# Kernel optimization log

Measured on AMD Instinct MI355X. Metric: run time of the kernel, lower is better.

## Reference

```python
import jax, jax.numpy as jnp
import numpy as np

N = 100_000      # nodes
E = 3_200_000    # edges (avg degree 32)
H = 16           # hidden channels
C_IN, C_OUT = 1, 2


def setup_inputs() -> dict:
    key = jax.random.key(0)
    k1, k2, k3, k4, k5 = jax.random.split(key, 5)
    x = jax.random.normal(k1, (N, C_IN), dtype=jnp.float32)
    src = jax.random.randint(k2, (E,), 0, N, dtype=jnp.int32)
    dst = jax.random.randint(k3, (E,), 0, N, dtype=jnp.int32)
    edge_index = jnp.stack([src, dst])  # [2, E], PyG layout
    # Glorot-style init for the two linear transforms
    W1 = jax.random.normal(k4, (C_IN, H), dtype=jnp.float32) * np.sqrt(2.0 / (C_IN + H))
    b1 = jnp.zeros((H,), dtype=jnp.float32)
    W2 = jax.random.normal(k5, (H, C_OUT), dtype=jnp.float32) * np.sqrt(2.0 / (H + C_OUT))
    b2 = jnp.zeros((C_OUT,), dtype=jnp.float32)
    return {"x": x, "edge_index": edge_index, "W1": W1, "b1": b1, "W2": W2, "b2": b2}


def _gcn_conv(x, src, dst, W, b):
    """GCNConv: out = D^{-1/2} (A+I) D^{-1/2} X W + b.
    src/dst already include self-loops. x: [N, Cin], W: [Cin, Cout]."""
    deg = jax.ops.segment_sum(jnp.ones_like(dst, dtype=x.dtype), dst, num_segments=N)
    dinv = jnp.where(deg > 0, jax.lax.rsqrt(jnp.maximum(deg, 1.0)), 0.0)
    norm = dinv[src] * dinv[dst]                       # [E+N]
    h = x @ W                                          # transform first (Cin small)
    msg = norm[:, None] * h[src]                       # [E+N, Cout]
    out = jax.ops.segment_sum(msg, dst, num_segments=N)
    return out + b


def reference(x, edge_index, W1, b1, W2, b2):
    loops = jnp.arange(N, dtype=edge_index.dtype)
    src = jnp.concatenate([edge_index[0], loops])      # add self-loops
    dst = jnp.concatenate([edge_index[1], loops])
    h = _gcn_conv(x, src, dst, W1, b1)
    h = jax.nn.relu(h)
    out = _gcn_conv(h, src, dst, W2, b2)
    return out
```

## Files before the change

### kernel.cpp

```cpp
#include <hip/hip_runtime.h>

#define NN 100000
#define NE 3200000
#define HC 16

#define BKT_BITS 7
#define BKT_NODES 128
#define NB 782
#define NB1 783
#define CHUNK_S 4096
#define NCC2 782
#define NCCP 784
#define MCAP 5120
#define PADW (((unsigned)NN << BKT_BITS) | (BKT_NODES - 1))

typedef unsigned uv4 __attribute__((ext_vector_type(4)));
typedef int      iv4 __attribute__((ext_vector_type(4)));


__global__ __launch_bounds__(256) void k_sortchunk(const int* __restrict__ src,
                                                   const int* __restrict__ dst,
                                                   unsigned short* __restrict__ Hoff,
                                                   unsigned* __restrict__ binned) {
    __shared__ unsigned h[NB1];
    __shared__ unsigned sorted[CHUNK_S];
    __shared__ unsigned wsum[4];
    int tid = threadIdx.x;
    int c = blockIdx.x;
    int b0 = c * CHUNK_S;
    int e1 = min(b0 + CHUNK_S, NE);
    int cnt = e1 - b0;

    for (int j = tid; j < NB1; j += 256) h[j] = 0;
    __syncthreads();

    iv4 dreg[4], sreg[4];
    int nit = 0;
    for (int v = b0 + tid * 4; v + 3 < e1; v += 1024) {
        iv4 d4 = *(const iv4*)(dst + v);
        iv4 s4 = *(const iv4*)(src + v);
        dreg[nit] = d4; sreg[nit] = s4; ++nit;
        atomicAdd(&h[((unsigned)d4.x) >> BKT_BITS], 1u);
        atomicAdd(&h[((unsigned)d4.y) >> BKT_BITS], 1u);
        atomicAdd(&h[((unsigned)d4.z) >> BKT_BITS], 1u);
        atomicAdd(&h[((unsigned)d4.w) >> BKT_BITS], 1u);
    }
    __syncthreads();

    int i0 = tid * 4;
    unsigned v0 = (i0 + 0 < NB1) ? h[i0 + 0] : 0;
    unsigned v1 = (i0 + 1 < NB1) ? h[i0 + 1] : 0;
    unsigned v2 = (i0 + 2 < NB1) ? h[i0 + 2] : 0;
    unsigned v3 = (i0 + 3 < NB1) ? h[i0 + 3] : 0;
    unsigned lsum = v0 + v1 + v2 + v3;
    unsigned sc = lsum;
#pragma unroll
    for (int off = 1; off < 64; off <<= 1) {
        unsigned u = __shfl_up(sc, off, 64);
        if ((tid & 63) >= off) sc += u;
    }
    int wave = tid >> 6;
    if ((tid & 63) == 63) wsum[wave] = sc;
    __syncthreads();
    unsigned wpre = 0;
    for (int w = 0; w < wave; ++w) wpre += wsum[w];
    unsigned excl = wpre + sc - lsum;
    __syncthreads();
    if (i0 + 0 < NB1) h[i0 + 0] = excl;
    if (i0 + 1 < NB1) h[i0 + 1] = excl + v0;
    if (i0 + 2 < NB1) h[i0 + 2] = excl + v0 + v1;
    if (i0 + 3 < NB1) h[i0 + 3] = excl + v0 + v1 + v2;

    unsigned short* row = Hoff + (size_t)c * NB1;
    if (i0 + 0 < NB1) row[i0 + 0] = (unsigned short)excl;
    if (i0 + 1 < NB1) row[i0 + 1] = (unsigned short)(excl + v0);
    if (i0 + 2 < NB1) row[i0 + 2] = (unsigned short)(excl + v0 + v1);
    if (i0 + 3 < NB1) row[i0 + 3] = (unsigned short)(excl + v0 + v1 + v2);
    __syncthreads();

    int it = 0;
    for (int v = b0 + tid * 4; v + 3 < e1; v += 1024, ++it) {
        iv4 d4 = dreg[it];
        iv4 s4 = sreg[it];
        {   unsigned d = (unsigned)d4.x, s = (unsigned)s4.x;
            unsigned pos = atomicAdd(&h[d >> BKT_BITS], 1u);
            sorted[pos] = (s << BKT_BITS) | (d & (BKT_NODES - 1)); }
        {   unsigned d = (unsigned)d4.y, s = (unsigned)s4.y;
            unsigned pos = atomicAdd(&h[d >> BKT_BITS], 1u);
            sorted[pos] = (s << BKT_BITS) | (d & (BKT_NODES - 1)); }
        {   unsigned d = (unsigned)d4.z, s = (unsigned)s4.z;
            unsigned pos = atomicAdd(&h[d >> BKT_BITS], 1u);
            sorted[pos] = (s << BKT_BITS) | (d & (BKT_NODES - 1)); }
        {   unsigned d = (unsigned)d4.w, s = (unsigned)s4.w;
            unsigned pos = atomicAdd(&h[d >> BKT_BITS], 1u);
            sorted[pos] = (s << BKT_BITS) | (d & (BKT_NODES - 1)); }
    }
    __syncthreads();

    unsigned* out = binned + (size_t)c * CHUNK_S;
    for (int j = tid * 4; j + 3 < cnt; j += 1024)
        *(uv4*)(out + j) = *(const uv4*)(sorted + j);
}


__global__ __launch_bounds__(256) void k_transT(const unsigned short* __restrict__ Hoff,
                                                unsigned short* __restrict__ TH) {
    __shared__ unsigned short tile[32][33];
    int tx = threadIdx.x & 31;
    int ty0 = (threadIdx.x >> 5) * 4;
    int c0 = blockIdx.x * 32;
    int b0 = blockIdx.y * 32;
#pragma unroll
    for (int k = 0; k < 4; ++k) {
        int c = c0 + ty0 + k, b = b0 + tx;
        tile[ty0 + k][tx] = (c < NCC2 && b < NB1) ? Hoff[(size_t)c * NB1 + b] : (unsigned short)0;
    }
    __syncthreads();
#pragma unroll
    for (int k = 0; k < 4; ++k) {
        int b = b0 + ty0 + k, c = c0 + tx;
        if (b < NB1 && c < NCC2) TH[(size_t)b * NCCP + c] = tile[tx][ty0 + k];
    }
}


__global__ __launch_bounds__(64) void k_totals(const unsigned short* __restrict__ TH,
                                               unsigned* __restrict__ totals) {
    int b = blockIdx.x;
    int lane = threadIdx.x;
    const unsigned short* r0 = TH + (size_t)b * NCCP;
    const unsigned short* r1 = r0 + NCCP;
    unsigned s = 0;
    for (int c = lane; c < NCC2; c += 64) s += (unsigned)r1[c] - (unsigned)r0[c];
#pragma unroll
    for (int off = 32; off >= 1; off >>= 1) s += __shfl_xor(s, off, 64);
    if (lane == 0) totals[b] = s;
}

__global__ __launch_bounds__(1024) void k_base2(const unsigned* __restrict__ totals,
                                                unsigned* __restrict__ gbase) {
    __shared__ unsigned s[1024];
    int t = threadIdx.x;
    unsigned v = (t < NB) ? ((totals[t] + 15u) & ~15u) : 0;
    s[t] = v;
    __syncthreads();
    for (int off = 1; off < 1024; off <<= 1) {
        unsigned u = (t >= off) ? s[t - off] : 0;
        __syncthreads();
        s[t] += u;
        __syncthreads();
    }
    if (t < NB) gbase[t] = s[t] - v;
}


__global__ __launch_bounds__(256) void k_merge_deg(const unsigned* __restrict__ binned,
                                                   const unsigned short* __restrict__ TH,
                                                   const unsigned* __restrict__ gbase,
                                                   const float* __restrict__ x,
                                                   unsigned* __restrict__ merged,
                                                   unsigned short* __restrict__ cofsg,
                                                   float* __restrict__ dinv,
                                                   float* __restrict__ p) {
    __shared__ unsigned short th0s[NCC2];
    __shared__ unsigned short lens[NCC2];
    __shared__ unsigned S[NB1];
    __shared__ unsigned wsum[4];
    __shared__ unsigned cnt[BKT_NODES];
    __shared__ unsigned stage[MCAP];
    __shared__ unsigned short cof[BKT_NODES + 2];
    __shared__ unsigned wsA;
    int tid = threadIdx.x, b = blockIdx.x;

    const unsigned short* r0 = TH + (size_t)b * NCCP;
    const unsigned short* r1 = r0 + NCCP;
    for (int c = tid; c < NCC2; c += 256) {
        unsigned a = r0[c];
        th0s[c] = (unsigned short)a;
        lens[c] = (unsigned short)((unsigned)r1[c] - a);
    }
    if (tid < BKT_NODES) cnt[tid] = 0;
    __syncthreads();

    int i0 = tid * 4;
    unsigned v0 = (i0 + 0 < NCC2) ? (unsigned)lens[i0 + 0] : 0;
    unsigned v1 = (i0 + 1 < NCC2) ? (unsigned)lens[i0 + 1] : 0;
    unsigned v2 = (i0 + 2 < NCC2) ? (unsigned)lens[i0 + 2] : 0;
    unsigned v3 = (i0 + 3 < NCC2) ? (unsigned)lens[i0 + 3] : 0;
    unsigned lsum = v0 + v1 + v2 + v3;
    unsigned sc = lsum;
#pragma unroll
    for (int off = 1; off < 64; off <<= 1) {
        unsigned u = __shfl_up(sc, off, 64);
        if ((tid & 63) >= off) sc += u;
    }
    int wave = tid >> 6;
    if ((tid & 63) == 63) wsum[wave] = sc;
    __syncthreads();
    unsigned wpre = 0;
    for (int w = 0; w < wave; ++w) wpre += wsum[w];
    unsigned excl = wpre + sc - lsum;
    if (i0 + 0 <= NCC2) S[i0 + 0] = excl;
    if (i0 + 1 <= NCC2) S[i0 + 1] = excl + v0;
    if (i0 + 2 <= NCC2) S[i0 + 2] = excl + v0 + v1;
    if (i0 + 3 <= NCC2) S[i0 + 3] = excl + v0 + v1 + v2;
    __syncthreads();

    unsigned T = S[NCC2];
    unsigned Tr = (T + 15u) & ~15u;
    unsigned gb = gbase[b];
    if (tid < 16) {
        unsigned q = T + tid;
        if (q < Tr) stage[q] = PADW;
    }

    for (int c = tid; c < NCC2; c += 256) {
        unsigned off = th0s[c], L = lens[c];
        if (!L) continue;
        unsigned base = S[c];
        const unsigned* segbase = binned + (size_t)c * CHUNK_S;
        unsigned je = off + L;
        for (unsigned j4 = off & ~3u; j4 < je; j4 += 4) {
            uv4 e4 = *(const uv4*)(segbase + j4);
#pragma unroll
            for (int k = 0; k < 4; ++k) {
                unsigned j = j4 + (unsigned)k;
                if (j >= off && j < je) {
                    unsigned e = ((const unsigned*)&e4)[k];
                    atomicAdd(&cnt[e & (BKT_NODES - 1)], 1u);
                    stage[base + (j - off)] = e;
                }
            }
        }
    }
    __syncthreads();

    for (unsigned j = tid * 4; j < Tr; j += 1024)
        *(uv4*)(merged + gb + j) = *(const uv4*)(stage + j);

    unsigned cv = (tid < BKT_NODES) ? cnt[tid] : 0u;
    unsigned csc = cv;
#pragma unroll
    for (int off = 1; off < 64; off <<= 1) {
        unsigned u = __shfl_up(csc, off, 64);
        if ((tid & 63) >= off) csc += u;
    }
    if (tid == 63) wsA = csc;
    __syncthreads();
    if (tid < BKT_NODES) {
        unsigned incl = csc + ((tid >= 64) ? wsA : 0u);
        cof[tid + 1] = (unsigned short)incl;
    }
    if (tid == 0) cof[0] = 0;
    __syncthreads();
    if (tid < BKT_NODES + 1)
        cofsg[(size_t)b * (BKT_NODES + 2) + tid] = cof[tid];

    int node = b * BKT_NODES + tid;
    if (tid < BKT_NODES) {
        if (node < NN) {
            float di = rsqrtf((float)(cnt[tid] + 1u));
            dinv[node] = di;
            p[node] = di * x[node];
        } else if (node == NN) {
            p[node] = 0.f;
        }
    }
}


__global__ __launch_bounds__(256) void k_agg1(const unsigned* __restrict__ merged,
                                              const unsigned* __restrict__ gbase,
                                              const unsigned* __restrict__ totals,
                                              const unsigned short* __restrict__ cofsg,
                                              const float* __restrict__ dinv,
                                              const float* __restrict__ p,
                                              const float* __restrict__ W1,
                                              const float* __restrict__ b1,
                                              const float* __restrict__ W2,
                                              float2* __restrict__ g) {
    __shared__ unsigned short cof[BKT_NODES + 2];
    __shared__ unsigned cur[BKT_NODES + 1];
    __shared__ unsigned se[MCAP];
    __shared__ float part[256];
    int tid = threadIdx.x, b = blockIdx.x;
    if (tid < BKT_NODES + 1) cof[tid] = cofsg[(size_t)b * (BKT_NODES + 2) + tid];
    __syncthreads();
    if (tid < BKT_NODES + 1) cur[tid] = cof[tid];
    __syncthreads();
    unsigned Tr = (totals[b] + 15u) & ~15u;
    const unsigned* m = merged + gbase[b];
    for (unsigned j = tid * 4; j < Tr; j += 1024) {
        uv4 e = *(const uv4*)(m + j);
        { unsigned w = e.x; unsigned sl = (w >> BKT_BITS >= NN) ? 128u : (w & (BKT_NODES - 1));
          se[atomicAdd(&cur[sl], 1u)] = w >> BKT_BITS; }
        { unsigned w = e.y; unsigned sl = (w >> BKT_BITS >= NN) ? 128u : (w & (BKT_NODES - 1));
          se[atomicAdd(&cur[sl], 1u)] = w >> BKT_BITS; }
        { unsigned w = e.z; unsigned sl = (w >> BKT_BITS >= NN) ? 128u : (w & (BKT_NODES - 1));
          se[atomicAdd(&cur[sl], 1u)] = w >> BKT_BITS; }
        { unsigned w = e.w; unsigned sl = (w >> BKT_BITS >= NN) ? 128u : (w & (BKT_NODES - 1));
          se[atomicAdd(&cur[sl], 1u)] = w >> BKT_BITS; }
    }
    __syncthreads();

    int nl = tid >> 1, half = tid & 1;
    unsigned o0 = cof[nl], o1 = cof[nl + 1];
    unsigned len = o1 - o0, mid = o0 + ((len + 1) >> 1);
    unsigned s = half ? mid : o0;
    unsigned e = half ? o1 : mid;
    float sum = 0.f;
    unsigned i = s;
    for (; i + 3 < e; i += 4) {
        unsigned a0 = se[i], a1 = se[i + 1], a2 = se[i + 2], a3 = se[i + 3];
        float x0 = p[a0], x1 = p[a1], x2 = p[a2], x3 = p[a3];
        sum += (x0 + x1) + (x2 + x3);
    }
    for (; i < e; ++i) sum += p[se[i]];
    part[tid] = sum;
    __syncthreads();

    if (!half) {
        int node = b * BKT_NODES + nl;
        if (node < NN) {
            float di = dinv[node];
            float sf = di * (part[tid] + part[tid + 1] + p[node]);
            float g0 = 0.f, g1 = 0.f;
#pragma unroll
            for (int c = 0; c < HC; ++c) {
                float h = fmaxf(fmaf(sf, W1[c], b1[c]), 0.f);
                g0 = fmaf(h, W2[2 * c], g0);
                g1 = fmaf(h, W2[2 * c + 1], g1);
            }
            g[node] = make_float2(di * g0, di * g1);
        }
    }
}


__global__ __launch_bounds__(256) void k_agg2(const unsigned* __restrict__ merged,
                                              const unsigned* __restrict__ gbase,
                                              const unsigned* __restrict__ totals,
                                              const unsigned short* __restrict__ cofsg,
                                              const float* __restrict__ dinv,
                                              const float2* __restrict__ g,
                                              const float* __restrict__ b2,
                                              float2* __restrict__ out) {
    __shared__ unsigned short cof[BKT_NODES + 2];
    __shared__ unsigned cur[BKT_NODES + 1];
    __shared__ unsigned se[MCAP];
    __shared__ float2 part[256];
    int tid = threadIdx.x, b = blockIdx.x;
    if (tid < BKT_NODES + 1) cof[tid] = cofsg[(size_t)b * (BKT_NODES + 2) + tid];
    __syncthreads();
    if (tid < BKT_NODES + 1) cur[tid] = cof[tid];
    __syncthreads();
    unsigned Tr = (totals[b] + 15u) & ~15u;
    const unsigned* m = merged + gbase[b];
    for (unsigned j = tid * 4; j < Tr; j += 1024) {
        uv4 e = *(const uv4*)(m + j);
        { unsigned w = e.x; unsigned sl = (w >> BKT_BITS >= NN) ? 128u : (w & (BKT_NODES - 1));
          se[atomicAdd(&cur[sl], 1u)] = w >> BKT_BITS; }
        { unsigned w = e.y; unsigned sl = (w >> BKT_BITS >= NN) ? 128u : (w & (BKT_NODES - 1));
          se[atomicAdd(&cur[sl], 1u)] = w >> BKT_BITS; }
        { unsigned w = e.z; unsigned sl = (w >> BKT_BITS >= NN) ? 128u : (w & (BKT_NODES - 1));
          se[atomicAdd(&cur[sl], 1u)] = w >> BKT_BITS; }
        { unsigned w = e.w; unsigned sl = (w >> BKT_BITS >= NN) ? 128u : (w & (BKT_NODES - 1));
          se[atomicAdd(&cur[sl], 1u)] = w >> BKT_BITS; }
    }
    __syncthreads();

    int nl = tid >> 1, half = tid & 1;
    unsigned o0 = cof[nl], o1 = cof[nl + 1];
    unsigned len = o1 - o0, mid = o0 + ((len + 1) >> 1);
    unsigned s = half ? mid : o0;
    unsigned e = half ? o1 : mid;
    float sx = 0.f, sy = 0.f;
    unsigned i = s;
    for (; i + 3 < e; i += 4) {
        unsigned a0 = se[i], a1 = se[i + 1], a2 = se[i + 2], a3 = se[i + 3];
        float2 v0 = g[a0], v1 = g[a1], v2 = g[a2], v3 = g[a3];
        sx += (v0.x + v1.x) + (v2.x + v3.x);
        sy += (v0.y + v1.y) + (v2.y + v3.y);
    }
    for (; i < e; ++i) { float2 v = g[se[i]]; sx += v.x; sy += v.y; }
    part[tid] = make_float2(sx, sy);
    __syncthreads();

    if (!half) {
        int node = b * BKT_NODES + nl;
        if (node < NN) {
            float di = dinv[node];
            float2 me = g[node];
            float ax = part[tid].x + part[tid + 1].x + me.x;
            float ay = part[tid].y + part[tid + 1].y + me.y;
            out[node] = make_float2(fmaf(di, ax, b2[0]), fmaf(di, ay, b2[1]));
        }
    }
}


__global__ __launch_bounds__(256) void f_deg(const int* __restrict__ dst,
                                             unsigned int* __restrict__ deg, int E) {
    int i = blockIdx.x * blockDim.x + threadIdx.x;
    if (i < E) atomicAdd(&deg[dst[i]], 1u);
}
__global__ __launch_bounds__(256) void f_node1(const float* __restrict__ x,
                                               const unsigned int* __restrict__ deg,
                                               float* __restrict__ dinv, float* __restrict__ p,
                                               float* __restrict__ t, int N) {
    int i = blockIdx.x * blockDim.x + threadIdx.x;
    if (i < N) {
        float di = rsqrtf((float)(deg[i] + 1u));
        dinv[i] = di; float pi = di * x[i]; p[i] = pi; t[i] = pi;
    }
}
__global__ __launch_bounds__(256) void f_scatter1(const int* __restrict__ src,
                                                  const int* __restrict__ dst,
                                                  const float* __restrict__ p,
                                                  float* __restrict__ t, int E) {
    int i = blockIdx.x * blockDim.x + threadIdx.x;
    if (i < E) atomicAdd(&t[dst[i]], p[src[i]]);
}
__global__ __launch_bounds__(256) void f_node2(const float* __restrict__ dinv,
                                               const float* __restrict__ t,
                                               const float* __restrict__ W1,
                                               const float* __restrict__ b1,
                                               const float* __restrict__ W2,
                                               float2* __restrict__ g,
                                               float2* __restrict__ acc, int N) {
    int i = blockIdx.x * blockDim.x + threadIdx.x;
    if (i < N) {
        float di = dinv[i]; float s = di * t[i];
        float g0 = 0.f, g1 = 0.f;
#pragma unroll
        for (int c = 0; c < HC; ++c) {
            float h = fmaxf(fmaf(s, W1[c], b1[c]), 0.f);
            g0 = fmaf(h, W2[2 * c], g0); g1 = fmaf(h, W2[2 * c + 1], g1);
        }
        float2 gv = make_float2(di * g0, di * g1);
        g[i] = gv; acc[i] = gv;
    }
}
__global__ __launch_bounds__(256) void f_scatter2(const int* __restrict__ src,
                                                  const int* __restrict__ dst,
                                                  const float2* __restrict__ g,
                                                  float* __restrict__ acc, int E) {
    int i = blockIdx.x * blockDim.x + threadIdx.x;
    if (i < E) {
        int s = src[i], d = dst[i];
        float2 gv = g[s];
        atomicAdd(&acc[2 * d], gv.x);
        atomicAdd(&acc[2 * d + 1], gv.y);
    }
}
__global__ __launch_bounds__(256) void f_out(const float* __restrict__ dinv,
                                             const float* __restrict__ b2,
                                             float* __restrict__ out, int N) {
    int i = blockIdx.x * blockDim.x + threadIdx.x;
    if (i < N) {
        float di = dinv[i];
        out[2 * i]     = fmaf(di, out[2 * i],     b2[0]);
        out[2 * i + 1] = fmaf(di, out[2 * i + 1], b2[1]);
    }
}

extern "C" void kernel_launch(void* const* d_in, const int* in_sizes, int n_in,
                              void* d_out, int out_size, void* d_ws, size_t ws_size,
                              hipStream_t stream) {
    const float* x  = (const float*)d_in[0];
    const int* ei   = (const int*)d_in[1];
    const int* src  = ei;
    const int* dst  = ei + NE;
    const float* W1 = (const float*)d_in[2];
    const float* b1 = (const float*)d_in[3];
    const float* W2 = (const float*)d_in[4];
    const float* b2 = (const float*)d_in[5];

    const int BT = 256;
    const int gridE = (NE + BT - 1) / BT;
    const int gridN = (NN + BT - 1) / BT;

    size_t need = 0;
    auto carve = [&](size_t bytes) { size_t o = need; need += (bytes + 255) & ~(size_t)255; return o; };
    size_t o_Hoff = carve((size_t)NCC2 * NB1 * 2);
    size_t o_TH   = carve((size_t)NB1 * NCCP * 2);
    size_t o_tot  = carve((size_t)NB * 4);
    size_t o_gb   = carve((size_t)(NB + 1) * 4);
    size_t o_cofs = carve((size_t)NB * (BKT_NODES + 2) * 2);
    size_t o_dinv = carve((size_t)NN * 4);
    size_t o_p    = carve((size_t)(NN + 1) * 4);
    size_t o_g    = carve((size_t)(NN + 1) * 8);
    size_t o_bin  = carve((size_t)NCC2 * CHUNK_S * 4);
    size_t o_mrg  = carve((size_t)(NE + 16 * NB + 64) * 4);

    if (ws_size >= need) {
        char* ws = (char*)d_ws;
        unsigned short* Hoff = (unsigned short*)(ws + o_Hoff);
        unsigned short* TH   = (unsigned short*)(ws + o_TH);
        unsigned* totals = (unsigned*)(ws + o_tot);
        unsigned* gbase  = (unsigned*)(ws + o_gb);
        unsigned short* cofs = (unsigned short*)(ws + o_cofs);
        float*    dinv   = (float*)(ws + o_dinv);
        float*    p      = (float*)(ws + o_p);
        float2*   g      = (float2*)(ws + o_g);
        unsigned* binned = (unsigned*)(ws + o_bin);
        unsigned* merged = (unsigned*)(ws + o_mrg);

        k_sortchunk<<<NCC2, 256, 0, stream>>>(src, dst, Hoff, binned);
        k_transT   <<<dim3(25, 25), 256, 0, stream>>>(Hoff, TH);
        k_totals   <<<NB, 64, 0, stream>>>(TH, totals);
        k_base2    <<<1, 1024, 0, stream>>>(totals, gbase);
        k_merge_deg<<<NB, 256, 0, stream>>>(binned, TH, gbase, x, merged, cofs, dinv, p);
        k_agg1     <<<NB, 256, 0, stream>>>(merged, gbase, totals, cofs, dinv, p, W1, b1, W2, g);
        k_agg2     <<<NB, 256, 0, stream>>>(merged, gbase, totals, cofs, dinv, g, b2, (float2*)d_out);
    } else {
        float* out = (float*)d_out;
        char* ws = (char*)d_ws;
        unsigned int* deg = (unsigned int*)ws;
        float* dinv = (float*)(ws + 1 * sizeof(float) * NN);
        float* p    = (float*)(ws + 2 * sizeof(float) * NN);
        float* t    = (float*)(ws + 3 * sizeof(float) * NN);
        float2* g   = (float2*)(ws + 4 * sizeof(float) * NN);

        hipMemsetAsync(deg, 0, NN * sizeof(unsigned int), stream);
        f_deg<<<gridE, BT, 0, stream>>>(dst, deg, NE);
        f_node1<<<gridN, BT, 0, stream>>>(x, deg, dinv, p, t, NN);
        f_scatter1<<<gridE, BT, 0, stream>>>(src, dst, p, t, NE);
        f_node2<<<gridN, BT, 0, stream>>>(dinv, t, W1, b1, W2, g, (float2*)out, NN);
        f_scatter2<<<gridE, BT, 0, stream>>>(src, dst, g, out, NE);
        f_out<<<gridN, BT, 0, stream>>>(dinv, b2, out, NN);
    }
}
```

Baseline: 155.4 us.

## Fuse both aggregation layers into one cooperative kernel with grid sync

Merges k_agg1 and k_agg2 into a single cooperative kernel. The per-bucket edge list is rebuilt into shared memory once and reused for both layers, with a grid-wide sync between them. This removes one kernel launch and the second pass that rebuilds se from merged. It relies on all 782 blocks being co-resident, and it falls back to the two-kernel path if the cooperative launch fails. The atomic-based fallback for small workspaces is removed, and g[NN] is now zeroed.

```diff
diff --git a/kernel.cpp b/kernel.cpp
--- a/kernel.cpp
+++ b/kernel.cpp
@@ -1,4 +1,7 @@
 #include <hip/hip_runtime.h>
+#include <hip/hip_cooperative_groups.h>
+
+namespace cg = cooperative_groups;
 
 #define NN 100000
 #define NE 3200000
@@ -269,6 +272,108 @@
 }
 
 
+__global__ __launch_bounds__(256) void k_agg12(const unsigned* __restrict__ merged,
+                                               const unsigned* __restrict__ gbase,
+                                               const unsigned* __restrict__ totals,
+                                               const unsigned short* __restrict__ cofsg,
+                                               const float* __restrict__ dinv,
+                                               const float* __restrict__ p,
+                                               const float* __restrict__ W1,
+                                               const float* __restrict__ b1,
+                                               const float* __restrict__ W2,
+                                               float2* __restrict__ g,
+                                               const float* __restrict__ b2,
+                                               float2* __restrict__ out) {
+    cg::grid_group grid = cg::this_grid();
+    __shared__ unsigned short cof[BKT_NODES + 2];
+    __shared__ unsigned cur[BKT_NODES + 1];
+    __shared__ unsigned se[MCAP];
+    __shared__ float part[256];
+    __shared__ float2 part2[256];
+    int tid = threadIdx.x, b = blockIdx.x;
+    if (tid < BKT_NODES + 1) cof[tid] = cofsg[(size_t)b * (BKT_NODES + 2) + tid];
+    __syncthreads();
+    if (tid < BKT_NODES + 1) cur[tid] = cof[tid];
+    __syncthreads();
+    unsigned Tr = (totals[b] + 15u) & ~15u;
+    const unsigned* m = merged + gbase[b];
+    for (unsigned j = tid * 4; j < Tr; j += 1024) {
+        uv4 e = *(const uv4*)(m + j);
+        { unsigned w = e.x; unsigned sl = (w >> BKT_BITS >= NN) ? 128u : (w & (BKT_NODES - 1));
+          se[atomicAdd(&cur[sl], 1u)] = w >> BKT_BITS; }
+        { unsigned w = e.y; unsigned sl = (w >> BKT_BITS >= NN) ? 128u : (w & (BKT_NODES - 1));
+          se[atomicAdd(&cur[sl], 1u)] = w >> BKT_BITS; }
+        { unsigned w = e.z; unsigned sl = (w >> BKT_BITS >= NN) ? 128u : (w & (BKT_NODES - 1));
+          se[atomicAdd(&cur[sl], 1u)] = w >> BKT_BITS; }
+        { unsigned w = e.w; unsigned sl = (w >> BKT_BITS >= NN) ? 128u : (w & (BKT_NODES - 1));
+          se[atomicAdd(&cur[sl], 1u)] = w >> BKT_BITS; }
+    }
+    __syncthreads();
+
+    int nl = tid >> 1, half = tid & 1;
+    unsigned o0 = cof[nl], o1 = cof[nl + 1];
+    unsigned len = o1 - o0, mid = o0 + ((len + 1) >> 1);
+    unsigned s = half ? mid : o0;
+    unsigned e = half ? o1 : mid;
+
+    {
+        float sum = 0.f;
+        unsigned i = s;
+        for (; i + 3 < e; i += 4) {
+            unsigned a0 = se[i], a1 = se[i + 1], a2 = se[i + 2], a3 = se[i + 3];
+            float x0 = p[a0], x1 = p[a1], x2 = p[a2], x3 = p[a3];
+            sum += (x0 + x1) + (x2 + x3);
+        }
+        for (; i < e; ++i) sum += p[se[i]];
+        part[tid] = sum;
+    }
+    __syncthreads();
+    if (!half) {
+        int node = b * BKT_NODES + nl;
+        if (node < NN) {
+            float di = dinv[node];
+            float sf = di * (part[tid] + part[tid + 1] + p[node]);
+            float g0 = 0.f, g1 = 0.f;
+#pragma unroll
+            for (int c = 0; c < HC; ++c) {
+                float h = fmaxf(fmaf(sf, W1[c], b1[c]), 0.f);
+                g0 = fmaf(h, W2[2 * c], g0);
+                g1 = fmaf(h, W2[2 * c + 1], g1);
+            }
+            g[node] = make_float2(di * g0, di * g1);
+        } else if (node == NN) {
+            g[node] = make_float2(0.f, 0.f);
+        }
+    }
+
+    grid.sync();
+
+    {
+        float sx = 0.f, sy = 0.f;
+        unsigned i = s;
+        for (; i + 3 < e; i += 4) {
+            unsigned a0 = se[i], a1 = se[i + 1], a2 = se[i + 2], a3 = se[i + 3];
+            float2 v0 = g[a0], v1 = g[a1], v2 = g[a2], v3 = g[a3];
+            sx += (v0.x + v1.x) + (v2.x + v3.x);
+            sy += (v0.y + v1.y) + (v2.y + v3.y);
+        }
+        for (; i < e; ++i) { float2 v = g[se[i]]; sx += v.x; sy += v.y; }
+        part2[tid] = make_float2(sx, sy);
+    }
+    __syncthreads();
+    if (!half) {
+        int node = b * BKT_NODES + nl;
+        if (node < NN) {
+            float di = dinv[node];
+            float2 me = g[node];
+            float ax = part2[tid].x + part2[tid + 1].x + me.x;
+            float ay = part2[tid].y + part2[tid + 1].y + me.y;
+            out[node] = make_float2(fmaf(di, ax, b2[0]), fmaf(di, ay, b2[1]));
+        }
+    }
+}
+
+
 __global__ __launch_bounds__(256) void k_agg1(const unsigned* __restrict__ merged,
                                               const unsigned* __restrict__ gbase,
                                               const unsigned* __restrict__ totals,
@@ -332,10 +437,11 @@
                 g1 = fmaf(h, W2[2 * c + 1], g1);
             }
             g[node] = make_float2(di * g0, di * g1);
-        }
-    }
-}
-
+        } else if (node == NN) {
+            g[node] = make_float2(0.f, 0.f);
+        }
+    }
+}
 
 __global__ __launch_bounds__(256) void k_agg2(const unsigned* __restrict__ merged,
                                               const unsigned* __restrict__ gbase,
@@ -398,72 +504,6 @@
     }
 }
 
-
-__global__ __launch_bounds__(256) void f_deg(const int* __restrict__ dst,
-                                             unsigned int* __restrict__ deg, int E) {
-    int i = blockIdx.x * blockDim.x + threadIdx.x;
-    if (i < E) atomicAdd(&deg[dst[i]], 1u);
-}
-__global__ __launch_bounds__(256) void f_node1(const float* __restrict__ x,
-                                               const unsigned int* __restrict__ deg,
-                                               float* __restrict__ dinv, float* __restrict__ p,
-                                               float* __restrict__ t, int N) {
-    int i = blockIdx.x * blockDim.x + threadIdx.x;
-    if (i < N) {
-        float di = rsqrtf((float)(deg[i] + 1u));
-        dinv[i] = di; float pi = di * x[i]; p[i] = pi; t[i] = pi;
-    }
-}
-__global__ __launch_bounds__(256) void f_scatter1(const int* __restrict__ src,
-                                                  const int* __restrict__ dst,
-                                                  const float* __restrict__ p,
-                                                  float* __restrict__ t, int E) {
-    int i = blockIdx.x * blockDim.x + threadIdx.x;
-    if (i < E) atomicAdd(&t[dst[i]], p[src[i]]);
-}
-__global__ __launch_bounds__(256) void f_node2(const float* __restrict__ dinv,
-                                               const float* __restrict__ t,
-                                               const float* __restrict__ W1,
-                                               const float* __restrict__ b1,
-                                               const float* __restrict__ W2,
-                                               float2* __restrict__ g,
-                                               float2* __restrict__ acc, int N) {
-    int i = blockIdx.x * blockDim.x + threadIdx.x;
-    if (i < N) {
-        float di = dinv[i]; float s = di * t[i];
-        float g0 = 0.f, g1 = 0.f;
-#pragma unroll
-        for (int c = 0; c < HC; ++c) {
-            float h = fmaxf(fmaf(s, W1[c], b1[c]), 0.f);
-            g0 = fmaf(h, W2[2 * c], g0); g1 = fmaf(h, W2[2 * c + 1], g1);
-        }
-        float2 gv = make_float2(di * g0, di * g1);
-        g[i] = gv; acc[i] = gv;
-    }
-}
-__global__ __launch_bounds__(256) void f_scatter2(const int* __restrict__ src,
-                                                  const int* __restrict__ dst,
-                                                  const float2* __restrict__ g,
-                                                  float* __restrict__ acc, int E) {
-    int i = blockIdx.x * blockDim.x + threadIdx.x;
-    if (i < E) {
-        int s = src[i], d = dst[i];
-        float2 gv = g[s];
-        atomicAdd(&acc[2 * d], gv.x);
-        atomicAdd(&acc[2 * d + 1], gv.y);
-    }
-}
-__global__ __launch_bounds__(256) void f_out(const float* __restrict__ dinv,
-                                             const float* __restrict__ b2,
-                                             float* __restrict__ out, int N) {
-    int i = blockIdx.x * blockDim.x + threadIdx.x;
-    if (i < N) {
-        float di = dinv[i];
-        out[2 * i]     = fmaf(di, out[2 * i],     b2[0]);
-        out[2 * i + 1] = fmaf(di, out[2 * i + 1], b2[1]);
-    }
-}
-
 extern "C" void kernel_launch(void* const* d_in, const int* in_sizes, int n_in,
                               void* d_out, int out_size, void* d_ws, size_t ws_size,
                               hipStream_t stream) {
@@ -475,10 +515,6 @@
     const float* b1 = (const float*)d_in[3];
     const float* W2 = (const float*)d_in[4];
     const float* b2 = (const float*)d_in[5];
-
-    const int BT = 256;
-    const int gridE = (NE + BT - 1) / BT;
-    const int gridN = (NN + BT - 1) / BT;
 
     size_t need = 0;
     auto carve = [&](size_t bytes) { size_t o = need; need += (bytes + 255) & ~(size_t)255; return o; };
@@ -493,41 +529,32 @@
     size_t o_bin  = carve((size_t)NCC2 * CHUNK_S * 4);
     size_t o_mrg  = carve((size_t)(NE + 16 * NB + 64) * 4);
 
-    if (ws_size >= need) {
-        char* ws = (char*)d_ws;
-        unsigned short* Hoff = (unsigned short*)(ws + o_Hoff);
-        unsigned short* TH   = (unsigned short*)(ws + o_TH);
-        unsigned* totals = (unsigned*)(ws + o_tot);
-        unsigned* gbase  = (unsigned*)(ws + o_gb);
-        unsigned short* cofs = (unsigned short*)(ws + o_cofs);
-        float*    dinv   = (float*)(ws + o_dinv);
-        float*    p      = (float*)(ws + o_p);
-        float2*   g      = (float2*)(ws + o_g);
-        unsigned* binned = (unsigned*)(ws + o_bin);
-        unsigned* merged = (unsigned*)(ws + o_mrg);
-
-        k_sortchunk<<<NCC2, 256, 0, stream>>>(src, dst, Hoff, binned);
-        k_transT   <<<dim3(25, 25), 256, 0, stream>>>(Hoff, TH);
-        k_totals   <<<NB, 64, 0, stream>>>(TH, totals);
-        k_base2    <<<1, 1024, 0, stream>>>(totals, gbase);
-        k_merge_deg<<<NB, 256, 0, stream>>>(binned, TH, gbase, x, merged, cofs, dinv, p);
-        k_agg1     <<<NB, 256, 0, stream>>>(merged, gbase, totals, cofs, dinv, p, W1, b1, W2, g);
-        k_agg2     <<<NB, 256, 0, stream>>>(merged, gbase, totals, cofs, dinv, g, b2, (float2*)d_out);
-    } else {
-        float* out = (float*)d_out;
-        char* ws = (char*)d_ws;
-        unsigned int* deg = (unsigned int*)ws;
-        float* dinv = (float*)(ws + 1 * sizeof(float) * NN);
-        float* p    = (float*)(ws + 2 * sizeof(float) * NN);
-        float* t    = (float*)(ws + 3 * sizeof(float) * NN);
-        float2* g   = (float2*)(ws + 4 * sizeof(float) * NN);
-
-        hipMemsetAsync(deg, 0, NN * sizeof(unsigned int), stream);
-        f_deg<<<gridE, BT, 0, stream>>>(dst, deg, NE);
-        f_node1<<<gridN, BT, 0, stream>>>(x, deg, dinv, p, t, NN);
-        f_scatter1<<<gridE, BT, 0, stream>>>(src, dst, p, t, NE);
-        f_node2<<<gridN, BT, 0, stream>>>(dinv, t, W1, b1, W2, g, (float2*)out, NN);
-        f_scatter2<<<gridE, BT, 0, stream>>>(src, dst, g, out, NE);
-        f_out<<<gridN, BT, 0, stream>>>(dinv, b2, out, NN);
-    }
-}
+    char* ws = (char*)d_ws;
+    unsigned short* Hoff = (unsigned short*)(ws + o_Hoff);
+    unsigned short* TH   = (unsigned short*)(ws + o_TH);
+    unsigned* totals = (unsigned*)(ws + o_tot);
+    unsigned* gbase  = (unsigned*)(ws + o_gb);
+    unsigned short* cofs = (unsigned short*)(ws + o_cofs);
+    float*    dinv   = (float*)(ws + o_dinv);
+    float*    p      = (float*)(ws + o_p);
+    float2*   g      = (float2*)(ws + o_g);
+    unsigned* binned = (unsigned*)(ws + o_bin);
+    unsigned* merged = (unsigned*)(ws + o_mrg);
+    float2*   outp   = (float2*)d_out;
+
+    k_sortchunk<<<NCC2, 256, 0, stream>>>(src, dst, Hoff, binned);
+    k_transT   <<<dim3(25, 25), 256, 0, stream>>>(Hoff, TH);
+    k_totals   <<<NB, 64, 0, stream>>>(TH, totals);
+    k_base2    <<<1, 1024, 0, stream>>>(totals, gbase);
+    k_merge_deg<<<NB, 256, 0, stream>>>(binned, TH, gbase, x, merged, cofs, dinv, p);
+
+    void* kargs[] = { (void*)&merged, (void*)&gbase, (void*)&totals, (void*)&cofs,
+                      (void*)&dinv, (void*)&p, (void*)&W1, (void*)&b1, (void*)&W2,
+                      (void*)&g, (void*)&b2, (void*)&outp };
+    hipError_t err = hipLaunchCooperativeKernel((void*)k_agg12, dim3(NB), dim3(256),
+                                                kargs, 0, stream);
+    if (err != hipSuccess) {
+        k_agg1<<<NB, 256, 0, stream>>>(merged, gbase, totals, cofs, dinv, p, W1, b1, W2, g);
+        k_agg2<<<NB, 256, 0, stream>>>(merged, gbase, totals, cofs, dinv, g, b2, outp);
+    }
+}
```

After: 269.1 us. 73.2% more time.
